# Kernel optimization log

Hardware: AMD Instinct MI355X
Metric: run time of the kernel (lower is better)

Reference implementation:

```python
import jax, jax.numpy as jnp
import numpy as np

N = 8192        # num_drugs
D_EMB = 256     # args.gcn_hidden3 (global encoder input)
D_FEAT = 256    # args.hidden_size (local encoder input)
H1 = H2 = H3 = 256  # args.ff_hidden1/2/3
LOG2 = float(np.log(2.0))
ADJ_DENSITY = 0.01


def _ff(x, w1, b1, w2, b2, w3, b3, ws, bs):
    # FF block: 3-layer ReLU MLP + linear shortcut (FF_local / FF_global)
    h = jax.nn.relu(x @ w1 + b1)
    h = jax.nn.relu(h @ w2 + b2)
    h = jax.nn.relu(h @ w3 + b3)
    return h + x @ ws + bs


def _lin_init(k, fan_in, fan_out):
    s = 1.0 / np.sqrt(fan_in)
    kw, kb = jax.random.split(k)
    w = jax.random.uniform(kw, (fan_in, fan_out), minval=-s, maxval=s, dtype=jnp.float32)
    b = jax.random.uniform(kb, (fan_out,), minval=-s, maxval=s, dtype=jnp.float32)
    return w, b


def setup_inputs() -> dict:
    key = jax.random.key(0)
    ks = jax.random.split(key, 11)
    g_w1, g_b1 = _lin_init(ks[0], D_EMB, H1)
    g_w2, g_b2 = _lin_init(ks[1], H1, H2)
    g_w3, g_b3 = _lin_init(ks[2], H2, H3)
    g_ws, g_bs = _lin_init(ks[3], D_EMB, H3)
    l_w1, l_b1 = _lin_init(ks[4], D_FEAT, H1)
    l_w2, l_b2 = _lin_init(ks[5], H1, H2)
    l_w3, l_b3 = _lin_init(ks[6], H2, H3)
    l_ws, l_bs = _lin_init(ks[7], D_FEAT, H3)
    embeddings = jax.random.normal(ks[8], (N, D_EMB), dtype=jnp.float32)
    features = jax.random.normal(ks[9], (N, D_FEAT), dtype=jnp.float32)
    adj_tensor = (jax.random.uniform(ks[10], (N, N)) < ADJ_DENSITY).astype(jnp.float32)
    return dict(embeddings=embeddings, features=features, adj_tensor=adj_tensor,
                num_drugs=N,
                g_w1=g_w1, g_b1=g_b1, g_w2=g_w2, g_b2=g_b2, g_w3=g_w3, g_b3=g_b3,
                g_ws=g_ws, g_bs=g_bs,
                l_w1=l_w1, l_b1=l_b1, l_w2=l_w2, l_b2=l_b2, l_w3=l_w3, l_b3=l_b3,
                l_ws=l_ws, l_bs=l_bs)


def reference(embeddings, features, adj_tensor,
              g_w1, g_b1, g_w2, g_b2, g_w3, g_b3, g_ws, g_bs,
              l_w1, l_b1, l_w2, l_b2, l_w3, l_b3, l_ws, l_bs,
              num_drugs):
    g_enc = _ff(embeddings, g_w1, g_b1, g_w2, g_b2, g_w3, g_b3, g_ws, g_bs)  # [N, H3]
    l_enc = _ff(features,   l_w1, l_b1, l_w2, l_b2, l_w3, l_b3, l_ws, l_bs)  # [N, H3]
    res = l_enc @ g_enc.T                      # [N, N] pairwise local-global scores
    pos_mask = adj_tensor
    neg_mask = 1.0 - adj_tensor
    # JSD estimator (as in InfoGraph/MIRACLE: mask applied BEFORE the expectation)
    p = res * pos_mask
    E_pos = jnp.sum(LOG2 - jax.nn.softplus(-p)) / num_drugs
    q = res * neg_mask
    E_neg = jnp.sum(jax.nn.softplus(-q) + q - LOG2) / (num_drugs * (num_drugs - 1))
    return E_neg - E_pos  # prior=False -> PRIOR term is 0
```

## Files before the change

kernel.cpp:

```cpp
#include <hip/hip_runtime.h>
#include <hip/hip_bf16.h>
#include <stdint.h>

typedef __bf16 bf16;
typedef __bf16 bf16x8 __attribute__((ext_vector_type(8)));
typedef float f32x4 __attribute__((ext_vector_type(4)));

#define N_DRUGS 8192
#define DIM 256
#define LOG2_C 0.6931471805599453f
#define W_POS (1.0f / 8192.0f)
#define W_NEG (1.0f / (8192.0f * 8191.0f))

__device__ inline void gload_lds16(const void* g, void* l) {
  __builtin_amdgcn_global_load_lds(
      (const __attribute__((address_space(1))) void*)g,
      (__attribute__((address_space(3))) void*)l, 16, 0, 0);
}

__device__ inline int swz(int row, int c) {
  return (c & ~7) | ((c ^ row) & 7);
}

__device__ inline float load_as_f32(const void* p, size_t idx, int dt_bf16) {
  return dt_bf16 ? (float)((const bf16*)p)[idx] : ((const float*)p)[idx];
}

__global__ void detect_dtype(const unsigned short* emb, int* flag) {
  int l = threadIdx.x & 63;
  unsigned short u = emb[2 * l];
  int e = (u >> 7) & 0xFF;
  int plausible = (e >= 96 && e <= 140) || (u == 0);
  unsigned long long m = __ballot(plausible);
  if (l == 0) *flag = (__popcll(m) >= 32) ? 1 : 0;
}

struct P8 { const void* p[8]; };

__global__ __launch_bounds__(256) void transpose_w(P8 srcs, bf16* wt,
                                                   const int* flag) {
  __shared__ bf16 t[32][33];
  const int dt = *flag;
  int m = blockIdx.z;
  const void* src = srcs.p[m];
  bf16* dst = wt + m * 65536;
  int bx = blockIdx.x * 32;
  int by = blockIdx.y * 32;
  int tx = threadIdx.x, ty = threadIdx.y;
#pragma unroll
  for (int i = 0; i < 32; i += 8)
    t[ty + i][tx] = (bf16)load_as_f32(src, (size_t)(by + ty + i) * DIM + bx + tx, dt);
  __syncthreads();
#pragma unroll
  for (int i = 0; i < 32; i += 8)
    dst[(bx + ty + i) * DIM + by + tx] = t[tx][ty + i];
}

struct FFArgs {
  const void *x, *b1, *b2, *b3, *bs;
  const bf16 *wt1, *wt2, *wt3, *wts;
  bf16* out;
};
struct FFBoth { FFArgs a[2]; };

__global__ __launch_bounds__(512) void ff_kernel(FFBoth both, const int* flag) {
  __shared__ __align__(16) bf16 xin[64 * 256];
  __shared__ __align__(16) bf16 cur[64 * 256];
  const FFArgs A = (blockIdx.y == 0) ? both.a[0] : both.a[1];
  const int dt = *flag;

  const int t = threadIdx.x;
  const int w = t >> 6, l = t & 63;
  const int lm = l & 15, lq = l >> 4;
  const int n0 = w * 32;
  const int r0 = blockIdx.x * 64;

  if (dt) {
#pragma unroll
    for (int it = 0; it < 4; ++it) {
      int ci = it * 512 + t, row = ci >> 5, c = ci & 31;
      *(bf16x8*)&xin[row * 256 + swz(row, c) * 8] =
          *(const bf16x8*)&((const bf16*)A.x)[(size_t)(r0 + row) * DIM + c * 8];
    }
  } else {
#pragma unroll
    for (int it = 0; it < 4; ++it) {
      int ci = it * 512 + t, row = ci >> 5, c = ci & 31;
      const float* src = &((const float*)A.x)[(size_t)(r0 + row) * DIM + c * 8];
      bf16x8 v;
#pragma unroll
      for (int e = 0; e < 8; ++e) v[e] = (bf16)src[e];
      *(bf16x8*)&xin[row * 256 + swz(row, c) * 8] = v;
    }
  }
  __syncthreads();

  f32x4 acc[4][2];
  const f32x4 fz = {0.f, 0.f, 0.f, 0.f};

  auto compute = [&](const bf16* src, const bf16* wt) {
#pragma unroll
    for (int i = 0; i < 4; ++i)
#pragma unroll
      for (int j = 0; j < 2; ++j) acc[i][j] = fz;
#pragma unroll
    for (int ks = 0; ks < 256; ks += 32) {
      bf16x8 af[4], bfr[2];
#pragma unroll
      for (int i = 0; i < 4; ++i) {
        int row = i * 16 + lm;
        af[i] = *(const bf16x8*)&src[row * 256 + swz(row, (ks >> 3) + lq) * 8];
      }
#pragma unroll
      for (int j = 0; j < 2; ++j) {
        int n = n0 + j * 16 + lm;
        bfr[j] = *(const bf16x8*)&wt[n * DIM + ks + lq * 8];
      }
#pragma unroll
      for (int i = 0; i < 4; ++i)
#pragma unroll
        for (int j = 0; j < 2; ++j)
          acc[i][j] = __builtin_amdgcn_mfma_f32_16x16x32_bf16(af[i], bfr[j],
                                                              acc[i][j], 0, 0, 0);
    }
  };

  auto store_relu = [&](const void* bias) {
    __syncthreads();
#pragma unroll
    for (int j = 0; j < 2; ++j) {
      int col = n0 + j * 16 + lm;
      float bj = load_as_f32(bias, col, dt);
      int cc = col >> 3, cw = col & 7;
#pragma unroll
      for (int i = 0; i < 4; ++i)
#pragma unroll
        for (int r = 0; r < 4; ++r) {
          int row = i * 16 + lq * 4 + r;
          float v = fmaxf(acc[i][j][r] + bj, 0.f);
          cur[row * 256 + swz(row, cc) * 8 + cw] = (bf16)v;
        }
    }
    __syncthreads();
  };

  compute(xin, A.wt1); store_relu(A.b1);
  compute(cur, A.wt2); store_relu(A.b2);
  compute(cur, A.wt3); store_relu(A.b3);
  compute(xin, A.wts);

  __syncthreads();
#pragma unroll
  for (int j = 0; j < 2; ++j) {
    int col = n0 + j * 16 + lm;
    float bj = load_as_f32(A.bs, col, dt);
    int cc = col >> 3, cw = col & 7;
#pragma unroll
    for (int i = 0; i < 4; ++i)
#pragma unroll
      for (int r = 0; r < 4; ++r) {
        int row = i * 16 + lq * 4 + r;
        float h3 = (float)cur[row * 256 + swz(row, cc) * 8 + cw];
        float v = acc[i][j][r] + bj + h3;
        xin[row * 256 + swz(row, cc) * 8 + cw] = (bf16)v;
      }
  }
  __syncthreads();
#pragma unroll
  for (int it = 0; it < 4; ++it) {
    int ci = it * 512 + t, row = ci >> 5, c = ci & 31;
    *(bf16x8*)&A.out[(size_t)(r0 + row) * DIM + c * 8] =
        *(const bf16x8*)&xin[row * 256 + swz(row, c) * 8];
  }
}

__global__ __launch_bounds__(256, 4) void gemm_reduce(const bf16* __restrict__ Lenc,
                                                      const bf16* __restrict__ Genc,
                                                      const void* __restrict__ adj,
                                                      float* accum, const int* flag) {
  __shared__ __align__(16) bf16 smem[2 * 128 * 64];
  __shared__ float red[4];
  bf16* At = smem;
  bf16* Bt = smem + 128 * 64;

  const int dt = *flag;
  const int t = threadIdx.x;
  const int w = t >> 6, l = t & 63;
  const int wr = w >> 1, wc = w & 1;
  const int lm = l & 15, lq = l >> 4;
  const int row0 = blockIdx.y * 128;
  const int col0 = blockIdx.x * 128;

  f32x4 acc[4][4];
  const f32x4 fz = {0.f, 0.f, 0.f, 0.f};
#pragma unroll
  for (int i = 0; i < 4; ++i)
#pragma unroll
    for (int j = 0; j < 4; ++j) acc[i][j] = fz;

  for (int kk = 0; kk < 256; kk += 64) {
    __syncthreads();
#pragma unroll
    for (int it = 0; it < 4; ++it) {
      int ci = it * 256 + t;
      int row = ci >> 3, cs = ci & 7;
      int cg = swz(row, cs);
      bf16* lbase = &At[(it * 256 + w * 64) * 8];
      gload_lds16(&Lenc[(size_t)(row0 + row) * DIM + kk + cg * 8], lbase);
      bf16* lbase2 = &Bt[(it * 256 + w * 64) * 8];
      gload_lds16(&Genc[(size_t)(col0 + row) * DIM + kk + cg * 8], lbase2);
    }
    __syncthreads();
#pragma unroll
    for (int ks = 0; ks < 64; ks += 32) {
      bf16x8 af[4], bfr[4];
#pragma unroll
      for (int i = 0; i < 4; ++i) {
        int row = wr * 64 + i * 16 + lm;
        af[i] = *(const bf16x8*)&At[row * 64 + swz(row, (ks >> 3) + lq) * 8];
      }
#pragma unroll
      for (int j = 0; j < 4; ++j) {
        int row = wc * 64 + j * 16 + lm;
        bfr[j] = *(const bf16x8*)&Bt[row * 64 + swz(row, (ks >> 3) + lq) * 8];
      }
#pragma unroll
      for (int i = 0; i < 4; ++i)
#pragma unroll
        for (int j = 0; j < 4; ++j)
          acc[i][j] = __builtin_amdgcn_mfma_f32_16x16x32_bf16(af[i], bfr[j],
                                                              acc[i][j], 0, 0, 0);
    }
  }

  __syncthreads();

  auto jsd = [&](float res, float a) {
    float s = fmaxf(res, 0.f) + __logf(1.f + __expf(-fabsf(res)));
    float vneg = (s - LOG2_C) * W_NEG;
    float vpos = (s - res - LOG2_C) * W_POS;
    return (a > 0.5f) ? vpos : vneg;
  };

  float lsum = 0.f;
  if (dt) {
    const bf16* gsrc = (const bf16*)adj +
        (size_t)(row0 + wr * 64) * N_DRUGS + col0 + wc * 64;
    bf16* wb = smem + w * 4096;
    int r8 = l >> 3, c8 = l & 7;
#pragma unroll
    for (int q = 0; q < 8; ++q)
      gload_lds16(gsrc + (size_t)(q * 8 + r8) * N_DRUGS + c8 * 8, wb + q * 512);
    asm volatile("s_waitcnt vmcnt(0)" ::: "memory");
    __builtin_amdgcn_sched_barrier(0);
#pragma unroll
    for (int i = 0; i < 4; ++i)
#pragma unroll
      for (int r = 0; r < 4; ++r) {
        int rc = i * 16 + lq * 4 + r;
#pragma unroll
        for (int j = 0; j < 4; ++j)
          lsum += jsd(acc[i][j][r], (float)wb[rc * 64 + j * 16 + lm]);
      }
  } else {
    const float* gsrc = (const float*)adj +
        (size_t)(row0 + wr * 64) * N_DRUGS + col0 + wc * 64;
    float* wfb = (float*)smem + w * 2048;
    auto issue = [&](int i) {
      float* cb = wfb + (i & 1) * 1024;
      const float* g = gsrc + (size_t)i * 16 * N_DRUGS;
#pragma unroll
      for (int q = 0; q < 4; ++q)
        gload_lds16(g + (size_t)(q * 4 + lq) * N_DRUGS + lm * 4, cb + q * 256);
    };
    issue(0);
    issue(1);
#pragma unroll
    for (int i = 0; i < 4; ++i) {
      if (i < 3) asm volatile("s_waitcnt vmcnt(4)" ::: "memory");
      else       asm volatile("s_waitcnt vmcnt(0)" ::: "memory");
      __builtin_amdgcn_sched_barrier(0);
      const float* cb = wfb + (i & 1) * 1024;
#pragma unroll
      for (int r = 0; r < 4; ++r) {
        int rc = lq * 4 + r;
#pragma unroll
        for (int j = 0; j < 4; ++j)
          lsum += jsd(acc[i][j][r], cb[rc * 64 + j * 16 + lm]);
      }
      if (i < 2) {
        asm volatile("s_waitcnt lgkmcnt(0)" ::: "memory");
        __builtin_amdgcn_sched_barrier(0);
        issue(i + 2);
      }
    }
  }

#pragma unroll
  for (int off = 32; off > 0; off >>= 1) lsum += __shfl_down(lsum, off, 64);
  if (l == 0) red[w] = lsum;
  __syncthreads();
  if (t == 0) atomicAdd(accum, red[0] + red[1] + red[2] + red[3]);
}

__global__ void finalize_k(const float* accum, unsigned int* out) {
  if (threadIdx.x == 0 && blockIdx.x == 0) {
    float v = *accum;
    union { bf16 h; unsigned short u; } cv;
    cv.h = (bf16)v;
    out[0] = ((unsigned int)cv.u << 16) | cv.u;
  }
}

extern "C" void kernel_launch(void* const* d_in, const int* in_sizes, int n_in,
                              void* d_out, int out_size, void* d_ws, size_t ws_size,
                              hipStream_t stream) {
  const void* embeddings = d_in[0];
  const void* features   = d_in[1];
  const void* adj        = d_in[2];

  char* ws = (char*)d_ws;
  float* accum = (float*)ws;
  int* flag = (int*)(ws + 64);
  bf16* wt   = (bf16*)(ws + 1024);
  bf16* genc = (bf16*)(ws + 1024 + 8 * 65536 * 2);
  bf16* lenc = (bf16*)(ws + 1024 + 8 * 65536 * 2 + (size_t)N_DRUGS * DIM * 2);

  hipMemsetAsync(accum, 0, sizeof(float), stream);

  detect_dtype<<<1, 64, 0, stream>>>((const unsigned short*)embeddings, flag);

  P8 srcs;
  srcs.p[0] = d_in[4];  srcs.p[1] = d_in[6];  srcs.p[2] = d_in[8];  srcs.p[3] = d_in[10];
  srcs.p[4] = d_in[12]; srcs.p[5] = d_in[14]; srcs.p[6] = d_in[16]; srcs.p[7] = d_in[18];
  transpose_w<<<dim3(8, 8, 8), dim3(32, 8), 0, stream>>>(srcs, wt, flag);

  FFBoth fb;
  fb.a[0] = FFArgs{embeddings, d_in[5], d_in[7], d_in[9], d_in[11],
                   wt + 0 * 65536, wt + 1 * 65536, wt + 2 * 65536, wt + 3 * 65536,
                   genc};
  fb.a[1] = FFArgs{features, d_in[13], d_in[15], d_in[17], d_in[19],
                   wt + 4 * 65536, wt + 5 * 65536, wt + 6 * 65536, wt + 7 * 65536,
                   lenc};
  ff_kernel<<<dim3(128, 2), 512, 0, stream>>>(fb, flag);

  gemm_reduce<<<dim3(64, 64), 256, 0, stream>>>(lenc, genc, adj, accum, flag);

  finalize_k<<<1, 64, 0, stream>>>(accum, (unsigned int*)d_out);
}
```

Measured before the change: 434.5 us.

## Restructure pairwise GEMM to 64x128 tiles with full-K LDS A and direct global B

The gemm_reduce kernel now uses 64x128 output tiles with twice as many blocks. Each block loads its whole 64x256 Lenc slice into LDS once, and each wave reads its Genc fragments straight from global memory, dropping the K-loop LDS staging and its barriers. The fp32 adjacency epilogue now loads each wave's 64x32 tile in one shot with an XOR-swizzled LDS layout instead of the double-buffered pipeline. The risks are more global traffic for Genc with no LDS reuse across waves, smaller per-wave MFMA tiles, and lost overlap in the adjacency loads.

```diff
diff --git a/kernel.cpp b/kernel.cpp
--- a/kernel.cpp
+++ b/kernel.cpp
@@ -178,59 +178,53 @@
                                                       const bf16* __restrict__ Genc,
                                                       const void* __restrict__ adj,
                                                       float* accum, const int* flag) {
-  __shared__ __align__(16) bf16 smem[2 * 128 * 64];
+  __shared__ __align__(16) bf16 At[64 * 256];
   __shared__ float red[4];
-  bf16* At = smem;
-  bf16* Bt = smem + 128 * 64;
 
   const int dt = *flag;
   const int t = threadIdx.x;
   const int w = t >> 6, l = t & 63;
-  const int wr = w >> 1, wc = w & 1;
   const int lm = l & 15, lq = l >> 4;
-  const int row0 = blockIdx.y * 128;
-  const int col0 = blockIdx.x * 128;
-
-  f32x4 acc[4][4];
+  const int row0 = blockIdx.x * 64;
+  const int col0 = blockIdx.y * 128;
+  const int wc0 = col0 + w * 32;
+
+#pragma unroll
+  for (int it = 0; it < 8; ++it) {
+    int ci = it * 256 + t;
+    int row = ci >> 5, c = ci & 31;
+    int cg = swz(row, c);
+    gload_lds16(&Lenc[(size_t)(row0 + row) * DIM + cg * 8],
+                &At[(it * 256 + w * 64) * 8]);
+  }
+  __syncthreads();
+
+  f32x4 acc[4][2];
   const f32x4 fz = {0.f, 0.f, 0.f, 0.f};
 #pragma unroll
   for (int i = 0; i < 4; ++i)
 #pragma unroll
-    for (int j = 0; j < 4; ++j) acc[i][j] = fz;
-
-  for (int kk = 0; kk < 256; kk += 64) {
-    __syncthreads();
-#pragma unroll
-    for (int it = 0; it < 4; ++it) {
-      int ci = it * 256 + t;
-      int row = ci >> 3, cs = ci & 7;
-      int cg = swz(row, cs);
-      bf16* lbase = &At[(it * 256 + w * 64) * 8];
-      gload_lds16(&Lenc[(size_t)(row0 + row) * DIM + kk + cg * 8], lbase);
-      bf16* lbase2 = &Bt[(it * 256 + w * 64) * 8];
-      gload_lds16(&Genc[(size_t)(col0 + row) * DIM + kk + cg * 8], lbase2);
-    }
-    __syncthreads();
-#pragma unroll
-    for (int ks = 0; ks < 64; ks += 32) {
-      bf16x8 af[4], bfr[4];
-#pragma unroll
-      for (int i = 0; i < 4; ++i) {
-        int row = wr * 64 + i * 16 + lm;
-        af[i] = *(const bf16x8*)&At[row * 64 + swz(row, (ks >> 3) + lq) * 8];
-      }
-#pragma unroll
-      for (int j = 0; j < 4; ++j) {
-        int row = wc * 64 + j * 16 + lm;
-        bfr[j] = *(const bf16x8*)&Bt[row * 64 + swz(row, (ks >> 3) + lq) * 8];
-      }
-#pragma unroll
-      for (int i = 0; i < 4; ++i)
-#pragma unroll
-        for (int j = 0; j < 4; ++j)
-          acc[i][j] = __builtin_amdgcn_mfma_f32_16x16x32_bf16(af[i], bfr[j],
-                                                              acc[i][j], 0, 0, 0);
-    }
+    for (int j = 0; j < 2; ++j) acc[i][j] = fz;
+
+#pragma unroll
+  for (int ks = 0; ks < 256; ks += 32) {
+    bf16x8 af[4], bfr[2];
+#pragma unroll
+    for (int i = 0; i < 4; ++i) {
+      int row = i * 16 + lm;
+      af[i] = *(const bf16x8*)&At[row * 256 + swz(row, (ks >> 3) + lq) * 8];
+    }
+#pragma unroll
+    for (int j = 0; j < 2; ++j) {
+      int n = wc0 + j * 16 + lm;
+      bfr[j] = *(const bf16x8*)&Genc[(size_t)n * DIM + ks + lq * 8];
+    }
+#pragma unroll
+    for (int i = 0; i < 4; ++i)
+#pragma unroll
+      for (int j = 0; j < 2; ++j)
+        acc[i][j] = __builtin_amdgcn_mfma_f32_16x16x32_bf16(af[i], bfr[j],
+                                                            acc[i][j], 0, 0, 0);
   }
 
   __syncthreads();
@@ -244,13 +238,14 @@
 
   float lsum = 0.f;
   if (dt) {
-    const bf16* gsrc = (const bf16*)adj +
-        (size_t)(row0 + wr * 64) * N_DRUGS + col0 + wc * 64;
-    bf16* wb = smem + w * 4096;
-    int r8 = l >> 3, c8 = l & 7;
-#pragma unroll
-    for (int q = 0; q < 8; ++q)
-      gload_lds16(gsrc + (size_t)(q * 8 + r8) * N_DRUGS + c8 * 8, wb + q * 512);
+    const bf16* gsrc = (const bf16*)adj + (size_t)row0 * N_DRUGS + wc0;
+    bf16* wb = At + w * 4096;
+#pragma unroll
+    for (int q = 0; q < 2; ++q) {
+      int ci = q * 64 + l;
+      int row = ci >> 1, c = ci & 1;
+      gload_lds16(gsrc + (size_t)row * N_DRUGS + c * 8, wb + q * 512);
+    }
     asm volatile("s_waitcnt vmcnt(0)" ::: "memory");
     __builtin_amdgcn_sched_barrier(0);
 #pragma unroll
@@ -259,41 +254,34 @@
       for (int r = 0; r < 4; ++r) {
         int rc = i * 16 + lq * 4 + r;
 #pragma unroll
-        for (int j = 0; j < 4; ++j)
-          lsum += jsd(acc[i][j][r], (float)wb[rc * 64 + j * 16 + lm]);
+        for (int j = 0; j < 2; ++j)
+          lsum += jsd(acc[i][j][r], (float)wb[rc * 32 + j * 16 + lm]);
       }
   } else {
-    const float* gsrc = (const float*)adj +
-        (size_t)(row0 + wr * 64) * N_DRUGS + col0 + wc * 64;
-    float* wfb = (float*)smem + w * 2048;
-    auto issue = [&](int i) {
-      float* cb = wfb + (i & 1) * 1024;
-      const float* g = gsrc + (size_t)i * 16 * N_DRUGS;
-#pragma unroll
-      for (int q = 0; q < 4; ++q)
-        gload_lds16(g + (size_t)(q * 4 + lq) * N_DRUGS + lm * 4, cb + q * 256);
-    };
-    issue(0);
-    issue(1);
-#pragma unroll
-    for (int i = 0; i < 4; ++i) {
-      if (i < 3) asm volatile("s_waitcnt vmcnt(4)" ::: "memory");
-      else       asm volatile("s_waitcnt vmcnt(0)" ::: "memory");
-      __builtin_amdgcn_sched_barrier(0);
-      const float* cb = wfb + (i & 1) * 1024;
+    const float* gsrc = (const float*)adj + (size_t)row0 * N_DRUGS + wc0;
+    float* wb = (float*)At + w * 2048;
+#pragma unroll
+    for (int q = 0; q < 8; ++q) {
+      int ci = q * 64 + l;
+      int row = ci >> 3, c = ci & 7;
+      int cg = c ^ (row & 7);
+      gload_lds16(gsrc + (size_t)row * N_DRUGS + cg * 4, wb + q * 256);
+    }
+    asm volatile("s_waitcnt vmcnt(0)" ::: "memory");
+    __builtin_amdgcn_sched_barrier(0);
+#pragma unroll
+    for (int i = 0; i < 4; ++i)
 #pragma unroll
       for (int r = 0; r < 4; ++r) {
-        int rc = lq * 4 + r;
-#pragma unroll
-        for (int j = 0; j < 4; ++j)
-          lsum += jsd(acc[i][j][r], cb[rc * 64 + j * 16 + lm]);
-      }
-      if (i < 2) {
-        asm volatile("s_waitcnt lgkmcnt(0)" ::: "memory");
-        __builtin_amdgcn_sched_barrier(0);
-        issue(i + 2);
-      }
-    }
+        int rc = i * 16 + lq * 4 + r;
+#pragma unroll
+        for (int j = 0; j < 2; ++j) {
+          int col = j * 16 + lm;
+          int slot = (col >> 2) ^ (rc & 7);
+          float a = wb[rc * 32 + slot * 4 + (col & 3)];
+          lsum += jsd(acc[i][j][r], a);
+        }
+      }
   }
 
 #pragma unroll
@@ -344,7 +332,7 @@
                    lenc};
   ff_kernel<<<dim3(128, 2), 512, 0, stream>>>(fb, flag);
 
-  gemm_reduce<<<dim3(64, 64), 256, 0, stream>>>(lenc, genc, adj, accum, flag);
+  gemm_reduce<<<dim3(128, 64), 256, 0, stream>>>(lenc, genc, adj, accum, flag);
 
   finalize_k<<<1, 64, 0, stream>>>(accum, (unsigned int*)d_out);
 }
```

New measurement: 469.2 us. +8.0%, slower.

## Double-buffer K-slices in gemm_reduce to overlap global loads with MFMA

Applied to the files above, without the earlier changes.

Replaces the single-buffered 64-wide K loop with eight 32-wide K slices in two LDS buffers. The next slice is prefetched with global_load_lds while MFMAs run on the current one, using vmcnt waits and raw s_barriers. LDS size stays the same. The cost is more barriers per tile and a new 4-chunk XOR swizzle that may change bank-conflict behaviour.

```diff
diff --git a/kernel.cpp b/kernel.cpp
--- a/kernel.cpp
+++ b/kernel.cpp
@@ -178,10 +178,8 @@
                                                       const bf16* __restrict__ Genc,
                                                       const void* __restrict__ adj,
                                                       float* accum, const int* flag) {
-  __shared__ __align__(16) bf16 smem[2 * 128 * 64];
+  __shared__ __align__(16) bf16 sb[2][2][128 * 32];
   __shared__ float red[4];
-  bf16* At = smem;
-  bf16* Bt = smem + 128 * 64;
 
   const int dt = *flag;
   const int t = threadIdx.x;
@@ -191,6 +189,19 @@
   const int row0 = blockIdx.y * 128;
   const int col0 = blockIdx.x * 128;
 
+  auto stage = [&](int buf, int k) {
+#pragma unroll
+    for (int q = 0; q < 2; ++q) {
+      int ci = q * 256 + t;
+      int row = ci >> 2, c = ci & 3;
+      int cg = c ^ (row & 3);
+      gload_lds16(&Lenc[(size_t)(row0 + row) * DIM + k * 32 + cg * 8],
+                  &sb[buf][0][(q * 256 + w * 64) * 8]);
+      gload_lds16(&Genc[(size_t)(col0 + row) * DIM + k * 32 + cg * 8],
+                  &sb[buf][1][(q * 256 + w * 64) * 8]);
+    }
+  };
+
   f32x4 acc[4][4];
   const f32x4 fz = {0.f, 0.f, 0.f, 0.f};
 #pragma unroll
@@ -198,42 +209,44 @@
 #pragma unroll
     for (int j = 0; j < 4; ++j) acc[i][j] = fz;
 
-  for (int kk = 0; kk < 256; kk += 64) {
-    __syncthreads();
-#pragma unroll
-    for (int it = 0; it < 4; ++it) {
-      int ci = it * 256 + t;
-      int row = ci >> 3, cs = ci & 7;
-      int cg = swz(row, cs);
-      bf16* lbase = &At[(it * 256 + w * 64) * 8];
-      gload_lds16(&Lenc[(size_t)(row0 + row) * DIM + kk + cg * 8], lbase);
-      bf16* lbase2 = &Bt[(it * 256 + w * 64) * 8];
-      gload_lds16(&Genc[(size_t)(col0 + row) * DIM + kk + cg * 8], lbase2);
-    }
-    __syncthreads();
-#pragma unroll
-    for (int ks = 0; ks < 64; ks += 32) {
-      bf16x8 af[4], bfr[4];
-#pragma unroll
-      for (int i = 0; i < 4; ++i) {
-        int row = wr * 64 + i * 16 + lm;
-        af[i] = *(const bf16x8*)&At[row * 64 + swz(row, (ks >> 3) + lq) * 8];
-      }
-#pragma unroll
-      for (int j = 0; j < 4; ++j) {
-        int row = wc * 64 + j * 16 + lm;
-        bfr[j] = *(const bf16x8*)&Bt[row * 64 + swz(row, (ks >> 3) + lq) * 8];
-      }
-#pragma unroll
-      for (int i = 0; i < 4; ++i)
-#pragma unroll
-        for (int j = 0; j < 4; ++j)
-          acc[i][j] = __builtin_amdgcn_mfma_f32_16x16x32_bf16(af[i], bfr[j],
-                                                              acc[i][j], 0, 0, 0);
-    }
-  }
-
-  __syncthreads();
+  auto compute = [&](int buf) {
+    bf16x8 af[4], bfr[4];
+#pragma unroll
+    for (int i = 0; i < 4; ++i) {
+      int row = wr * 64 + i * 16 + lm;
+      af[i] = *(const bf16x8*)&sb[buf][0][row * 32 + (lq ^ (row & 3)) * 8];
+    }
+#pragma unroll
+    for (int j = 0; j < 4; ++j) {
+      int row = wc * 64 + j * 16 + lm;
+      bfr[j] = *(const bf16x8*)&sb[buf][1][row * 32 + (lq ^ (row & 3)) * 8];
+    }
+#pragma unroll
+    for (int i = 0; i < 4; ++i)
+#pragma unroll
+      for (int j = 0; j < 4; ++j)
+        acc[i][j] = __builtin_amdgcn_mfma_f32_16x16x32_bf16(af[i], bfr[j],
+                                                            acc[i][j], 0, 0, 0);
+  };
+
+  stage(0, 0);
+#pragma unroll
+  for (int k = 0; k < 8; ++k) {
+    const int cur = k & 1;
+    if (k < 7) {
+      stage(cur ^ 1, k + 1);
+      asm volatile("s_waitcnt vmcnt(4)" ::: "memory");
+    } else {
+      asm volatile("s_waitcnt vmcnt(0)" ::: "memory");
+    }
+    __builtin_amdgcn_sched_barrier(0);
+    __builtin_amdgcn_s_barrier();
+    asm volatile("" ::: "memory");
+    compute(cur);
+    asm volatile("" ::: "memory");
+    __builtin_amdgcn_s_barrier();
+    asm volatile("" ::: "memory");
+  }
 
   auto jsd = [&](float res, float a) {
     float s = fmaxf(res, 0.f) + __logf(1.f + __expf(-fabsf(res)));
@@ -246,7 +259,7 @@
   if (dt) {
     const bf16* gsrc = (const bf16*)adj +
         (size_t)(row0 + wr * 64) * N_DRUGS + col0 + wc * 64;
-    bf16* wb = smem + w * 4096;
+    bf16* wb = (bf16*)sb + w * 4096;
     int r8 = l >> 3, c8 = l & 7;
 #pragma unroll
     for (int q = 0; q < 8; ++q)
@@ -265,7 +278,7 @@
   } else {
     const float* gsrc = (const float*)adj +
         (size_t)(row0 + wr * 64) * N_DRUGS + col0 + wc * 64;
-    float* wfb = (float*)smem + w * 2048;
+    float* wfb = (float*)sb + w * 2048;
     auto issue = [&](int i) {
       float* cb = wfb + (i & 1) * 1024;
       const float* g = gsrc + (size_t)i * 16 * N_DRUGS;
```

Result: no change. 439.9 us (+1.2%).
